# Optimization experiments

Measured on AMD Instinct MI355X. Metric: run time of the kernel, lower is better.

Reference implementation:

```python
import jax, jax.numpy as jnp
import numpy as np

N = 8192


def setup_inputs() -> dict:
    key = jax.random.key(0)
    k1, k2 = jax.random.split(key)
    pos = jax.random.uniform(k1, (N, 2), dtype=jnp.float32)          # nn.init.uniform_ on [N,2] param
    dist = jax.random.uniform(k2, (N, N), dtype=jnp.float32)         # target graph distances [N,N]
    return {"pos": pos, "dist": dist}


def reference(pos, dist):
    # pairwise differences: [N, N, 2]  (broadcasted1 - broadcasted2 in torch code)
    diff = pos[None, :, :] - pos[:, None, :]
    sq = jnp.sum(diff * diff, axis=-1)                               # [N, N]
    # safe sqrt: torch.norm has subgradient 0 at 0 (diagonal); guard to stay grad-safe
    pred_dist = jnp.where(sq > 0, jnp.sqrt(jnp.where(sq > 0, sq, 1.0)), 0.0)
    mask = dist != 0
    pred_dist = jnp.where(mask, pred_dist, dist)
    safe_dist = jnp.where(mask, dist, 1.0)                           # avoid 0-division; masked anyway
    stress_matrix = jnp.where(mask, jnp.square((pred_dist - dist) / safe_dist), dist)
    return jnp.sum(stress_matrix)
```

## Files before the change

### kernel.cpp

```cpp
#include <hip/hip_runtime.h>

#define NDIM 8192
#define ROWS_PER_BLOCK 4
#define BLOCK 256

__global__ __launch_bounds__(BLOCK) void stress_sum_kernel(
    const float* __restrict__ pos,
    const float* __restrict__ dist,
    float* __restrict__ out)
{
    const int row0 = blockIdx.x * ROWS_PER_BLOCK;

    float pix[ROWS_PER_BLOCK], piy[ROWS_PER_BLOCK];
#pragma unroll
    for (int r = 0; r < ROWS_PER_BLOCK; ++r) {
        pix[r] = pos[2 * (row0 + r)];
        piy[r] = pos[2 * (row0 + r) + 1];
    }

    float acc = 0.0f;

    for (int jb = threadIdx.x * 4; jb < NDIM; jb += BLOCK * 4) {
        const float4 p01 = *(const float4*)(pos + 2 * jb);
        const float4 p23 = *(const float4*)(pos + 2 * jb + 4);
        const float pjx[4] = {p01.x, p01.z, p23.x, p23.z};
        const float pjy[4] = {p01.y, p01.w, p23.y, p23.w};

#pragma unroll
        for (int r = 0; r < ROWS_PER_BLOCK; ++r) {
            const float4 d4 =
                *(const float4*)(dist + (size_t)(row0 + r) * NDIM + jb);
            const float dv[4] = {d4.x, d4.y, d4.z, d4.w};
#pragma unroll
            for (int k = 0; k < 4; ++k) {
                const float dx = pjx[k] - pix[r];
                const float dy = pjy[k] - piy[r];
                const float sq = dx * dx + dy * dy;
                const float pred = sqrtf(sq);
                const float d = dv[k];
                const float rcp = __builtin_amdgcn_rcpf(d);
                const float t = pred * rcp - 1.0f;
                acc += (d != 0.0f) ? t * t : 0.0f;
            }
        }
    }

#pragma unroll
    for (int off = 32; off > 0; off >>= 1)
        acc += __shfl_down(acc, off, 64);

    __shared__ float wave_sums[BLOCK / 64];
    const int lane = threadIdx.x & 63;
    const int wave = threadIdx.x >> 6;
    if (lane == 0) wave_sums[wave] = acc;
    __syncthreads();

    if (threadIdx.x == 0) {
        float s = 0.0f;
#pragma unroll
        for (int w = 0; w < BLOCK / 64; ++w) s += wave_sums[w];
        atomicAdd(out, s);
    }
}

extern "C" void kernel_launch(void* const* d_in, const int* in_sizes, int n_in,
                              void* d_out, int out_size, void* d_ws, size_t ws_size,
                              hipStream_t stream)
{
    const float* pos  = (const float*)d_in[0];
    const float* dist = (const float*)d_in[1];
    float* out = (float*)d_out;

    hipMemsetAsync(out, 0, sizeof(float) * out_size, stream);

    const int grid = NDIM / ROWS_PER_BLOCK;
    stress_sum_kernel<<<grid, BLOCK, 0, stream>>>(pos, dist, out);
}
```

Baseline: 360.3 us.

## Widen per-thread column tiles and replace atomics with two-pass reduction

```diff
diff --git a/kernel.cpp b/kernel.cpp
--- a/kernel.cpp
+++ b/kernel.cpp
@@ -3,11 +3,13 @@
 #define NDIM 8192
 #define ROWS_PER_BLOCK 4
 #define BLOCK 256
+#define GRID (NDIM / ROWS_PER_BLOCK)
+#define COLS_PER_THREAD 8
 
-__global__ __launch_bounds__(BLOCK) void stress_sum_kernel(
+__global__ __launch_bounds__(BLOCK) void stress_partial_kernel(
     const float* __restrict__ pos,
     const float* __restrict__ dist,
-    float* __restrict__ out)
+    float* __restrict__ partials)
 {
     const int row0 = blockIdx.x * ROWS_PER_BLOCK;
 
@@ -20,19 +22,24 @@
 
     float acc = 0.0f;
 
-    for (int jb = threadIdx.x * 4; jb < NDIM; jb += BLOCK * 4) {
-        const float4 p01 = *(const float4*)(pos + 2 * jb);
-        const float4 p23 = *(const float4*)(pos + 2 * jb + 4);
-        const float pjx[4] = {p01.x, p01.z, p23.x, p23.z};
-        const float pjy[4] = {p01.y, p01.w, p23.y, p23.w};
+    for (int jb = threadIdx.x * COLS_PER_THREAD; jb < NDIM; jb += BLOCK * COLS_PER_THREAD) {
+        float pjx[COLS_PER_THREAD], pjy[COLS_PER_THREAD];
+#pragma unroll
+        for (int q = 0; q < 4; ++q) {
+            const float4 p = *(const float4*)(pos + 2 * jb + 4 * q);
+            pjx[2 * q]     = p.x;  pjy[2 * q]     = p.y;
+            pjx[2 * q + 1] = p.z;  pjy[2 * q + 1] = p.w;
+        }
 
 #pragma unroll
         for (int r = 0; r < ROWS_PER_BLOCK; ++r) {
-            const float4 d4 =
-                *(const float4*)(dist + (size_t)(row0 + r) * NDIM + jb);
-            const float dv[4] = {d4.x, d4.y, d4.z, d4.w};
+            const float* drow = dist + (size_t)(row0 + r) * NDIM + jb;
+            const float4 d0 = *(const float4*)(drow);
+            const float4 d1 = *(const float4*)(drow + 4);
+            const float dv[COLS_PER_THREAD] = {d0.x, d0.y, d0.z, d0.w,
+                                               d1.x, d1.y, d1.z, d1.w};
 #pragma unroll
-            for (int k = 0; k < 4; ++k) {
+            for (int k = 0; k < COLS_PER_THREAD; ++k) {
                 const float dx = pjx[k] - pix[r];
                 const float dy = pjy[k] - piy[r];
                 const float sq = dx * dx + dy * dy;
@@ -59,7 +66,34 @@
         float s = 0.0f;
 #pragma unroll
         for (int w = 0; w < BLOCK / 64; ++w) s += wave_sums[w];
-        atomicAdd(out, s);
+        partials[blockIdx.x] = s;
+    }
+}
+
+__global__ __launch_bounds__(BLOCK) void reduce_final_kernel(
+    const float* __restrict__ partials,
+    float* __restrict__ out)
+{
+    float acc = 0.0f;
+#pragma unroll
+    for (int i = 0; i < GRID / BLOCK; ++i)
+        acc += partials[threadIdx.x + i * BLOCK];
+
+#pragma unroll
+    for (int off = 32; off > 0; off >>= 1)
+        acc += __shfl_down(acc, off, 64);
+
+    __shared__ float wave_sums[BLOCK / 64];
+    const int lane = threadIdx.x & 63;
+    const int wave = threadIdx.x >> 6;
+    if (lane == 0) wave_sums[wave] = acc;
+    __syncthreads();
+
+    if (threadIdx.x == 0) {
+        float s = 0.0f;
+#pragma unroll
+        for (int w = 0; w < BLOCK / 64; ++w) s += wave_sums[w];
+        out[0] = s;
     }
 }
 
@@ -70,9 +104,8 @@
     const float* pos  = (const float*)d_in[0];
     const float* dist = (const float*)d_in[1];
     float* out = (float*)d_out;
+    float* partials = (float*)d_ws;
 
-    hipMemsetAsync(out, 0, sizeof(float) * out_size, stream);
-
-    const int grid = NDIM / ROWS_PER_BLOCK;
-    stress_sum_kernel<<<grid, BLOCK, 0, stream>>>(pos, dist, out);
+    stress_partial_kernel<<<GRID, BLOCK, 0, stream>>>(pos, dist, partials);
+    reduce_final_kernel<<<1, BLOCK, 0, stream>>>(partials, out);
 }
```

Measured after the change: 353.6 us, median of 2. No clear change (-1.9%).
